# Optimization experiments

Hardware: AMD Instinct MI355X
Metric: run time of the kernel (lower is better)

The kernel has to match this reference:

```python
import jax, jax.numpy as jnp
import numpy as np

WD, WH, WW = 2, 7, 7          # window size (D, H, W)
SD, SH, SW = 1, 3, 3          # shift size
NUM_HEADS = 3
DIM = 96
N = WD * WH * WW              # tokens per window = 98


def _rel_pos_index():
    coords = np.stack(np.meshgrid(np.arange(WD), np.arange(WH), np.arange(WW), indexing='ij'))
    flat = coords.reshape(3, -1)                                   # (3, N)
    rel = (flat[:, :, None] - flat[:, None, :]).transpose(1, 2, 0)  # (N, N, 3)
    rel[..., 0] += WD - 1
    rel[..., 1] += WH - 1
    rel[..., 2] += WW - 1
    rel[..., 0] *= (2 * WH - 1) * (2 * WW - 1)
    rel[..., 1] *= (2 * WW - 1)
    return rel.sum(-1)                                             # (N, N) int


def _attn_mask(D, H, W):
    # shifted-window mask as in compute_mask(); purely shape-dependent constant
    img = np.zeros((D, H, W), np.float32)
    cnt = 0
    for d in (slice(-WD), slice(-WD, -SD), slice(-SD, None)):
        for h in (slice(-WH), slice(-WH, -SH), slice(-SH, None)):
            for w in (slice(-WW), slice(-WW, -SW), slice(-SW, None)):
                img[d, h, w] = cnt
                cnt += 1
    mw = img.reshape(D // WD, WD, H // WH, WH, W // WW, WW)
    mw = mw.transpose(0, 2, 4, 1, 3, 5).reshape(-1, N)             # (nW, N)
    diff = mw[:, None, :] - mw[:, :, None]
    return np.where(diff != 0, np.float32(-100.0), np.float32(0.0))  # (nW, N, N)


def _layernorm(x, w, b, eps=1e-5):
    mu = x.mean(-1, keepdims=True)
    var = ((x - mu) ** 2).mean(-1, keepdims=True)
    return (x - mu) * jax.lax.rsqrt(var + eps) * w + b


def _window_partition(x):
    B, D, H, W, C = x.shape
    x = x.reshape(B, D // WD, WD, H // WH, WH, W // WW, WW, C)
    return x.transpose(0, 1, 3, 5, 2, 4, 6, 7).reshape(-1, N, C)


def _window_reverse(win, B, D, H, W):
    C = win.shape[-1]
    x = win.reshape(B, D // WD, H // WH, W // WW, WD, WH, WW, C)
    return x.transpose(0, 1, 4, 2, 5, 3, 6, 7).reshape(B, D, H, W, C)


def swin_block(x, norm1_w, norm1_b, qkv_w, qkv_b, rpb_table, proj_w, proj_b,
               norm2_w, norm2_b, fc1_w, fc1_b, fc2_w, fc2_b):
    B, D, H, W, C = x.shape
    hd = C // NUM_HEADS
    shortcut = x
    # W-MSA (shifted) branch
    h = _layernorm(x, norm1_w, norm1_b)
    h = jnp.roll(h, shift=(-SD, -SH, -SW), axis=(1, 2, 3))
    win = _window_partition(h)                                     # (B*nW, N, C)
    qkv = win @ qkv_w.T + qkv_b                                    # (B*nW, N, 3C)
    qkv = qkv.reshape(-1, N, 3, NUM_HEADS, hd).transpose(2, 0, 3, 1, 4)
    q = qkv[0] * (hd ** -0.5)
    k, v = qkv[1], qkv[2]                                          # (B*nW, nh, N, hd)
    attn = jnp.einsum('whnd,whmd->whnm', q, k)                     # (B*nW, nh, N, N)
    rpi = jnp.asarray(_rel_pos_index().reshape(-1))
    bias = rpb_table[rpi].reshape(N, N, NUM_HEADS).transpose(2, 0, 1)
    attn = attn + bias[None]
    mask = jnp.asarray(_attn_mask(D, H, W))                        # (nW, N, N)
    nW = mask.shape[0]
    attn = attn.reshape(B, nW, NUM_HEADS, N, N) + mask[None, :, None]
    attn = jax.nn.softmax(attn.reshape(-1, NUM_HEADS, N, N), axis=-1)
    out = jnp.einsum('whnm,whmd->whnd', attn, v)                   # (B*nW, nh, N, hd)
    out = out.transpose(0, 2, 1, 3).reshape(-1, N, C)
    out = out @ proj_w.T + proj_b
    out = _window_reverse(out, B, D, H, W)
    out = jnp.roll(out, shift=(SD, SH, SW), axis=(1, 2, 3))
    x = shortcut + out
    # MLP branch
    h2 = _layernorm(x, norm2_w, norm2_b)
    h2 = jax.nn.gelu(h2 @ fc1_w.T + fc1_b, approximate=False) @ fc2_w.T + fc2_b
    return x + h2


def setup_inputs() -> dict:
    key = jax.random.key(0)
    ks = jax.random.split(key, 8)
    C, HID = DIM, 4 * DIM
    return {
        'x': jax.random.normal(ks[0], (2, 8, 112, 112, C), jnp.float32),
        'norm1_w': jnp.ones((C,), jnp.float32),
        'norm1_b': jnp.zeros((C,), jnp.float32),
        'qkv_w': jax.random.normal(ks[1], (3 * C, C), jnp.float32) * 0.02,
        'qkv_b': jnp.zeros((3 * C,), jnp.float32),
        'rpb_table': jax.random.normal(ks[2], ((2 * WD - 1) * (2 * WH - 1) * (2 * WW - 1), NUM_HEADS), jnp.float32) * 0.02,
        'proj_w': jax.random.normal(ks[3], (C, C), jnp.float32) * 0.02,
        'proj_b': jnp.zeros((C,), jnp.float32),
        'norm2_w': jnp.ones((C,), jnp.float32),
        'norm2_b': jnp.zeros((C,), jnp.float32),
        'fc1_w': jax.random.normal(ks[4], (HID, C), jnp.float32) * 0.02,
        'fc1_b': jnp.zeros((HID,), jnp.float32),
        'fc2_w': jax.random.normal(ks[5], (C, HID), jnp.float32) * 0.02,
        'fc2_b': jnp.zeros((C,), jnp.float32),
    }


def reference(x, norm1_w, norm1_b, qkv_w, qkv_b, rpb_table, proj_w, proj_b,
              norm2_w, norm2_b, fc1_w, fc1_b, fc2_w, fc2_b):
    return swin_block(x, norm1_w, norm1_b, qkv_w, qkv_b, rpb_table, proj_w, proj_b,
                      norm2_w, norm2_b, fc1_w, fc1_b, fc2_w, fc2_b)
```

## Files before the change

### kernel.cpp

```cpp
#include <hip/hip_runtime.h>
#include <hip/hip_bf16.h>


typedef __bf16 bf16x8 __attribute__((ext_vector_type(8)));
typedef __bf16 bf16x4 __attribute__((ext_vector_type(4)));
typedef float f32x4 __attribute__((ext_vector_type(4)));

#define SCALE_Q 0.17677669529663687f
#define LOG2E   1.4426950408889634f
#define SCALE_QE (SCALE_Q * LOG2E)

static __device__ __forceinline__ f32x4 mfma16(bf16x8 a, bf16x8 b, f32x4 c) {
  return __builtin_amdgcn_mfma_f32_16x16x32_bf16(a, b, c, 0, 0, 0);
}

static __device__ __forceinline__ float fast_exp2(float x) {
#if __has_builtin(__builtin_amdgcn_exp2f)
  return __builtin_amdgcn_exp2f(x);
#else
  return exp2f(x);
#endif
}
static __device__ __forceinline__ float fast_rcp(float x) {
#if __has_builtin(__builtin_amdgcn_rcpf)
  return __builtin_amdgcn_rcpf(x);
#else
  return 1.f / x;
#endif
}

static __device__ __forceinline__ float fast_gelu(float x) {
  float e = fast_exp2(x * fmaf(-0.1029445213f, x * x, -2.3022077385f));
  return x * fast_rcp(1.f + e);
}

static __device__ __forceinline__ int src_tok(int wi, int n) {
  int b = wi >> 10, r = wi & 1023;
  int d0 = r >> 8, h0 = (r >> 4) & 15, w0 = r & 15;
  int dd = n / 49, rem = n - dd * 49, hh = rem / 7, ww = rem - hh * 7;
  int d = (d0 * 2 + dd + 1) & 7;
  int h = h0 * 7 + hh + 3; if (h >= 112) h -= 112;
  int w = w0 * 7 + ww + 3; if (w >= 112) w -= 112;
  return ((b * 8 + d) * 112 + h) * 112 + w;
}

static __device__ __forceinline__ int region_cls(int cls, int n) {
  int dd = n / 49, rem = n - dd * 49, hh = rem / 7, ww = rem - hh * 7;
  int dr = (cls & 4) ? dd + 1 : 0;
  int hr = (cls & 2) ? (hh < 4 ? 1 : 2) : 0;
  int wr = (cls & 1) ? (ww < 4 ? 1 : 2) : 0;
  return dr * 9 + hr * 3 + wr;
}

__global__ __launch_bounds__(256) void k0_prep(
    const float* __restrict__ qkv_w, const float* __restrict__ qkv_b,
    const float* __restrict__ rpb, const float* __restrict__ proj_w,
    const float* __restrict__ fc1_w, const float* __restrict__ fc2_w,
    __bf16* __restrict__ wqkv, float* __restrict__ qkvb_s,
    __bf16* __restrict__ wproj, __bf16* __restrict__ wfc1, __bf16* __restrict__ wfc2,
    float* __restrict__ biasF) {
  int idx = blockIdx.x * 256 + threadIdx.x;
  if (idx < 27648) {
    int row = idx / 96; float v = qkv_w[idx];
    wqkv[idx] = (__bf16)(row < 96 ? v * SCALE_QE : v); return;
  }
  idx -= 27648;
  if (idx < 9216) { wproj[idx] = (__bf16)proj_w[idx]; return; }
  idx -= 9216;
  if (idx < 36864) { wfc1[idx] = (__bf16)fc1_w[idx]; return; }
  idx -= 36864;
  if (idx < 36864) { wfc2[idx] = (__bf16)fc2_w[idx]; return; }
  idx -= 36864;
  if (idx < 288) { float v = qkv_b[idx]; qkvb_s[idx] = idx < 96 ? v * SCALE_QE : v; return; }
  idx -= 288;
  if (idx < 301056) {
    int j = idx & 3, lane = (idx >> 2) & 63, t = idx >> 8;
    int nt = t % 7, mt = (t / 7) % 7, hd = (t / 49) % 3, cls = t / 147;
    int i = 16 * mt + 4 * (lane >> 4) + j;
    int jt = 16 * nt + (lane & 15);
    float v;
    if (jt >= 98) {
      v = -1e30f;
    } else {
      float rp = 0.f;
      if (i < 98) {
        int di = i / 49, ri_ = i - di * 49, hi = ri_ / 7, wi_ = ri_ - hi * 7;
        int dj = jt / 49, rj_ = jt - dj * 49, hj = rj_ / 7, wj = rj_ - hj * 7;
        int rpi = (di - dj + 1) * 169 + (hi - hj + 6) * 13 + (wi_ - wj + 6);
        rp = rpb[rpi * 3 + hd];
      }
      float mk = (region_cls(cls, i) != region_cls(cls, jt)) ? -100.f : 0.f;
      v = (rp + mk) * LOG2E;
    }
    biasF[idx] = v;
  }
}

__global__ __launch_bounds__(512, 1) void k1234_attn(
    const float* __restrict__ x, const float* __restrict__ n1w, const float* __restrict__ n1b,
    const __bf16* __restrict__ wqkv, const float* __restrict__ qkvb,
    const f32x4* __restrict__ biasF, const __bf16* __restrict__ wproj,
    const float* __restrict__ projb, float* __restrict__ x2) {
  int wi = blockIdx.x;
  int tid = threadIdx.x;
  int wave = tid >> 6, l = tid & 63, col = l & 15, gq = l >> 4;
  __shared__ __bf16 win_lds[112][104];
  __shared__ __bf16 Q_lds[112][104];
  __shared__ __bf16 K_lds[112][104];
  __shared__ __bf16 Vt_lds[96][136];
  __shared__ __bf16 p_lds[8][16][136];

  if (tid < 392) {
    int row = tid >> 2, cq = (tid & 3) * 24;
    const float* src = x + (size_t)src_tok(wi, row) * 96 + cq;
    float v[24];
    float sm = 0.f, sq = 0.f;
#pragma unroll
    for (int i = 0; i < 6; i++) {
      f32x4 u = *(const f32x4*)(src + 4 * i);
#pragma unroll
      for (int k = 0; k < 4; k++) { v[4 * i + k] = u[k]; sm += u[k]; sq += u[k] * u[k]; }
    }
    sm += __shfl_xor(sm, 1); sq += __shfl_xor(sq, 1);
    sm += __shfl_xor(sm, 2); sq += __shfl_xor(sq, 2);
    float mean = sm * (1.f / 96.f);
    float rstd = rsqrtf(sq * (1.f / 96.f) - mean * mean + 1e-5f);
    __bf16 outv[24];
#pragma unroll
    for (int i = 0; i < 24; i++)
      outv[i] = (__bf16)((v[i] - mean) * rstd * n1w[cq + i] + n1b[cq + i]);
#pragma unroll
    for (int i = 0; i < 3; i++)
      *(bf16x8*)&win_lds[row][cq + 8 * i] = *(bf16x8*)&outv[8 * i];
  } else {
    int z = tid - 392;
    for (int e = z; e < 1344; e += 120) { int r = e / 96; win_lds[98 + r][e - r * 96] = (__bf16)0.f; }
    for (int e = z; e < 1536; e += 120) Vt_lds[e >> 4][112 + (e & 15)] = (__bf16)0.f;
  }
  __syncthreads();

  if (wave < 6) {
    f32x4 acc[7][3] = {};
#pragma unroll
    for (int kk = 0; kk < 3; kk++) {
      bf16x8 a[7], bb[3];
#pragma unroll
      for (int mt = 0; mt < 7; mt++)
        a[mt] = *(const bf16x8*)&win_lds[16 * mt + col][32 * kk + 8 * gq];
#pragma unroll
      for (int t = 0; t < 3; t++)
        bb[t] = *(const bf16x8*)(wqkv + (size_t)(wave * 48 + 16 * t + col) * 96 + 32 * kk + 8 * gq);
#pragma unroll
      for (int mt = 0; mt < 7; mt++)
#pragma unroll
        for (int t = 0; t < 3; t++) acc[mt][t] = mfma16(a[mt], bb[t], acc[mt][t]);
    }
#pragma unroll
    for (int t = 0; t < 3; t++) {
      int n = wave * 48 + 16 * t + col;
      float bias = qkvb[n];
      int which = n / 96, c = n - which * 96;
      if (which == 2) {
#pragma unroll
        for (int mt = 0; mt < 7; mt++) {
          bf16x4 pk;
#pragma unroll
          for (int j = 0; j < 4; j++) pk[j] = (__bf16)(acc[mt][t][j] + bias);
          *(bf16x4*)&Vt_lds[c][16 * mt + 4 * gq] = pk;
        }
      } else {
#pragma unroll
        for (int mt = 0; mt < 7; mt++) {
#pragma unroll
          for (int j = 0; j < 4; j++) {
            int row = 16 * mt + 4 * gq + j;
            float v = acc[mt][t][j] + bias;
            if (which == 0) Q_lds[row][c] = (__bf16)v;
            else            K_lds[row][c] = (__bf16)v;
          }
        }
      }
    }
  }
  __syncthreads();

  {
    {
      int rr = l >> 2, cc = 112 + ((l & 3) << 2);
      *(uint2*)&p_lds[wave][rr][cc] = make_uint2(0u, 0u);
    }
    int cls = ((((wi >> 8) & 3) == 3) ? 4 : 0) | ((((wi >> 4) & 15) == 15) ? 2 : 0) |
              (((wi & 15) == 15) ? 1 : 0);
    int ntiles = (wave < 6) ? 3 : (wave == 6 ? 2 : 1);
    bf16x8 kf[7], vf[2][4];
    int cur_hd = -1;
#pragma unroll 1
    for (int s = 0; s < ntiles; s++) {
      int hd, mt;
      if (wave < 6)      { hd = wave >> 1; mt = ((wave & 1) ? 4 : 0) + s; }
      else if (wave == 6){ hd = s;         mt = 3; }
      else               { hd = 2;         mt = 3; }
      if (hd != cur_hd) {
        cur_hd = hd;
#pragma unroll
        for (int nt = 0; nt < 7; nt++)
          kf[nt] = *(const bf16x8*)&K_lds[16 * nt + col][hd * 32 + 8 * gq];
#pragma unroll
        for (int nt = 0; nt < 2; nt++)
#pragma unroll
          for (int ks = 0; ks < 4; ks++)
            vf[nt][ks] = *(const bf16x8*)&Vt_lds[hd * 32 + 16 * nt + col][32 * ks + 8 * gq];
      }
      const f32x4* bfr = biasF + (size_t)((cls * 3 + hd) * 49) * 64 + l;
      bf16x8 qf = *(const bf16x8*)&Q_lds[16 * mt + col][hd * 32 + 8 * gq];
      float sum0 = 0.f, sum1 = 0.f, sum2 = 0.f, sum3 = 0.f;
#pragma unroll
      for (int nt = 0; nt < 7; nt++) {
        f32x4 sv = mfma16(qf, kf[nt], bfr[(mt * 7 + nt) * 64]);
        float e0 = fast_exp2(sv[0]); sum0 += e0;
        float e1 = fast_exp2(sv[1]); sum1 += e1;
        float e2 = fast_exp2(sv[2]); sum2 += e2;
        float e3 = fast_exp2(sv[3]); sum3 += e3;
        p_lds[wave][4 * gq + 0][16 * nt + col] = (__bf16)e0;
        p_lds[wave][4 * gq + 1][16 * nt + col] = (__bf16)e1;
        p_lds[wave][4 * gq + 2][16 * nt + col] = (__bf16)e2;
        p_lds[wave][4 * gq + 3][16 * nt + col] = (__bf16)e3;
      }
#pragma unroll
      for (int m = 1; m < 16; m <<= 1) {
        sum0 += __shfl_xor(sum0, m, 16);
        sum1 += __shfl_xor(sum1, m, 16);
        sum2 += __shfl_xor(sum2, m, 16);
        sum3 += __shfl_xor(sum3, m, 16);
      }
      f32x4 oacc0 = {}, oacc1 = {};
#pragma unroll
      for (int ks = 0; ks < 4; ks++) {
        bf16x8 pa = *(const bf16x8*)&p_lds[wave][col][32 * ks + 8 * gq];
        oacc0 = mfma16(pa, vf[0][ks], oacc0);
        oacc1 = mfma16(pa, vf[1][ks], oacc1);
      }
      float inv0 = fast_rcp(sum0), inv1 = fast_rcp(sum1), inv2 = fast_rcp(sum2), inv3 = fast_rcp(sum3);
      int ibase = 16 * mt + 4 * gq;
      win_lds[ibase + 0][hd * 32 + col]      = (__bf16)(oacc0[0] * inv0);
      win_lds[ibase + 1][hd * 32 + col]      = (__bf16)(oacc0[1] * inv1);
      win_lds[ibase + 2][hd * 32 + col]      = (__bf16)(oacc0[2] * inv2);
      win_lds[ibase + 3][hd * 32 + col]      = (__bf16)(oacc0[3] * inv3);
      win_lds[ibase + 0][hd * 32 + 16 + col] = (__bf16)(oacc1[0] * inv0);
      win_lds[ibase + 1][hd * 32 + 16 + col] = (__bf16)(oacc1[1] * inv1);
      win_lds[ibase + 2][hd * 32 + 16 + col] = (__bf16)(oacc1[2] * inv2);
      win_lds[ibase + 3][hd * 32 + 16 + col] = (__bf16)(oacc1[3] * inv3);
    }
  }
  __syncthreads();

  if (wave < 6) {
    f32x4 acc[7] = {};
#pragma unroll
    for (int kk = 0; kk < 3; kk++) {
      bf16x8 bb = *(const bf16x8*)(wproj + (size_t)(16 * wave + col) * 96 + 32 * kk + 8 * gq);
#pragma unroll
      for (int mt = 0; mt < 7; mt++) {
        bf16x8 a = *(const bf16x8*)&win_lds[16 * mt + col][32 * kk + 8 * gq];
        acc[mt] = mfma16(a, bb, acc[mt]);
      }
    }
    int c = 16 * wave + col;
    float pb = projb[c];
#pragma unroll
    for (int mt = 0; mt < 7; mt++) {
#pragma unroll
      for (int j = 0; j < 4; j++) {
        int i = 16 * mt + 4 * gq + j;
        if (i < 98) {
          size_t s = (size_t)src_tok(wi, i);
          x2[s * 96 + c] = x[s * 96 + c] + acc[mt][j] + pb;
        }
      }
    }
  }
}

__global__ __launch_bounds__(512, 2) void k567_mlp(
    const float* __restrict__ n2w, const float* __restrict__ n2b,
    const __bf16* __restrict__ wfc1, const float* __restrict__ fc1b,
    const __bf16* __restrict__ wfc2, const float* __restrict__ fc2b,
    float* __restrict__ x2) {
  int tid = threadIdx.x;
  int wave = tid >> 6, l = tid & 63, col = l & 15, gq = l >> 4;
  size_t rowbase = (size_t)blockIdx.x * 128 + wave * 16;
  __shared__ __bf16 wbuf[2][96][104];
  __shared__ __bf16 htl[8][16][104];

  bf16x8 afr[3];
  {
    float v[24];
    float sm = 0.f, sq = 0.f;
    const float* src = x2 + (rowbase + col) * 96 + 8 * gq;
#pragma unroll
    for (int kk = 0; kk < 3; kk++) {
      f32x4 u0 = *(const f32x4*)(src + 32 * kk);
      f32x4 u1 = *(const f32x4*)(src + 32 * kk + 4);
#pragma unroll
      for (int k = 0; k < 4; k++) {
        v[8 * kk + k] = u0[k];     sm += u0[k]; sq += u0[k] * u0[k];
        v[8 * kk + 4 + k] = u1[k]; sm += u1[k]; sq += u1[k] * u1[k];
      }
    }
    sm += __shfl_xor(sm, 16); sq += __shfl_xor(sq, 16);
    sm += __shfl_xor(sm, 32); sq += __shfl_xor(sq, 32);
    float mean = sm * (1.f / 96.f);
    float rstd = rsqrtf(sq * (1.f / 96.f) - mean * mean + 1e-5f);
#pragma unroll
    for (int kk = 0; kk < 3; kk++) {
      f32x4 w0 = *(const f32x4*)(n2w + 32 * kk + 8 * gq);
      f32x4 w1 = *(const f32x4*)(n2w + 32 * kk + 8 * gq + 4);
      f32x4 b0 = *(const f32x4*)(n2b + 32 * kk + 8 * gq);
      f32x4 b1 = *(const f32x4*)(n2b + 32 * kk + 8 * gq + 4);
#pragma unroll
      for (int k = 0; k < 4; k++) {
        afr[kk][k]     = (__bf16)((v[8 * kk + k]     - mean) * rstd * w0[k] + b0[k]);
        afr[kk][4 + k] = (__bf16)((v[8 * kk + 4 + k] - mean) * rstd * w1[k] + b1[k]);
      }
    }
  }

#define STAGE_LOAD(qq, st)                                                        \
  {                                                                               \
    _Pragma("unroll")                                                             \
    for (int i = 0; i < 4; i++) {                                                 \
      int u = tid + 512 * i;                                                      \
      int which = u >= 1152; int uu = u - which * 1152;                           \
      int row = uu / 12, c = uu - row * 12;                                       \
      const __bf16* g = which ? (wfc2 + (size_t)row * 384 + (qq) * 96 + c * 8)    \
                              : (wfc1 + ((size_t)((qq) * 96 + row)) * 96 + c * 8);\
      st[i] = *(const bf16x8*)g;                                                  \
    }                                                                             \
    if (tid < 256) {                                                              \
      int u = 2048 + tid;                                                         \
      int row = (u - 1152) / 12, c = (u - 1152) - row * 12;                       \
      st[4] = *(const bf16x8*)(wfc2 + (size_t)row * 384 + (qq) * 96 + c * 8);     \
    }                                                                             \
  }
#define STAGE_WRITE(st)                                                           \
  {                                                                               \
    _Pragma("unroll")                                                             \
    for (int i = 0; i < 4; i++) {                                                 \
      int u = tid + 512 * i;                                                      \
      int which = u >= 1152; int uu = u - which * 1152;                           \
      int row = uu / 12, c = uu - row * 12;                                       \
      *(bf16x8*)&wbuf[which][row][c * 8] = st[i];                                 \
    }                                                                             \
    if (tid < 256) {                                                              \
      int u = 2048 + tid;                                                         \
      int row = (u - 1152) / 12, c = (u - 1152) - row * 12;                       \
      *(bf16x8*)&wbuf[1][row][c * 8] = st[4];                                     \
    }                                                                             \
  }

  {
    bf16x8 st[5];
    STAGE_LOAD(0, st);
    STAGE_WRITE(st);
  }
  __syncthreads();

  f32x4 oc[6] = {};
#pragma unroll 1
  for (int q = 0; q < 4; q++) {
    bf16x8 st[5];
    if (q < 3) STAGE_LOAD(q + 1, st);
    f32x4 acc[6] = {};
#pragma unroll
    for (int kk = 0; kk < 3; kk++) {
      bf16x8 bb[6];
#pragma unroll
      for (int t = 0; t < 6; t++)
        bb[t] = *(const bf16x8*)&wbuf[0][16 * t + col][32 * kk + 8 * gq];
#pragma unroll
      for (int t = 0; t < 6; t++) acc[t] = mfma16(afr[kk], bb[t], acc[t]);
    }
#pragma unroll
    for (int t = 0; t < 6; t++) {
      float bv = fc1b[q * 96 + 16 * t + col];
#pragma unroll
      for (int j = 0; j < 4; j++)
        htl[wave][4 * gq + j][16 * t + col] = (__bf16)fast_gelu(acc[t][j] + bv);
    }
#pragma unroll
    for (int kk = 0; kk < 3; kk++) {
      bf16x8 a0 = *(const bf16x8*)&htl[wave][col][32 * kk + 8 * gq];
      bf16x8 bb[6];
#pragma unroll
      for (int t = 0; t < 6; t++)
        bb[t] = *(const bf16x8*)&wbuf[1][16 * t + col][32 * kk + 8 * gq];
#pragma unroll
      for (int t = 0; t < 6; t++) oc[t] = mfma16(a0, bb[t], oc[t]);
    }
    __syncthreads();
    if (q < 3) {
      STAGE_WRITE(st);
      __syncthreads();
    }
  }
#pragma unroll
  for (int t = 0; t < 6; t++) {
    float bv = fc2b[16 * t + col];
#pragma unroll
    for (int j = 0; j < 4; j++) {
      size_t row = rowbase + 4 * gq + j;
      x2[row * 96 + 16 * t + col] = x2[row * 96 + 16 * t + col] + oc[t][j] + bv;
    }
  }
#undef STAGE_LOAD
#undef STAGE_WRITE
}

#define O_WQKV   0L
#define O_WPROJ  55296L
#define O_WFC1   73728L
#define O_WFC2   147456L
#define O_QKVB   221184L
#define O_BIASF  222336L

extern "C" void kernel_launch(void* const* d_in, const int* in_sizes, int n_in,
                              void* d_out, int out_size, void* d_ws, size_t ws_size,
                              hipStream_t stream) {
  const float* x     = (const float*)d_in[0];
  const float* n1w   = (const float*)d_in[1];
  const float* n1b   = (const float*)d_in[2];
  const float* qkvw  = (const float*)d_in[3];
  const float* qkvb  = (const float*)d_in[4];
  const float* rpb   = (const float*)d_in[5];
  const float* projw = (const float*)d_in[6];
  const float* projb = (const float*)d_in[7];
  const float* n2w   = (const float*)d_in[8];
  const float* n2b   = (const float*)d_in[9];
  const float* fc1w  = (const float*)d_in[10];
  const float* fc1b  = (const float*)d_in[11];
  const float* fc2w  = (const float*)d_in[12];
  const float* fc2b  = (const float*)d_in[13];

  char* ws = (char*)d_ws;
  __bf16* wqkv   = (__bf16*)(ws + O_WQKV);
  __bf16* wproj  = (__bf16*)(ws + O_WPROJ);
  __bf16* wfc1   = (__bf16*)(ws + O_WFC1);
  __bf16* wfc2   = (__bf16*)(ws + O_WFC2);
  float*  qkvb_s = (float*)(ws + O_QKVB);
  float*  biasF  = (float*)(ws + O_BIASF);
  float*  x2     = (float*)d_out;

  k0_prep<<<1610, 256, 0, stream>>>(qkvw, qkvb, rpb, projw, fc1w, fc2w,
                                    wqkv, qkvb_s, wproj, wfc1, wfc2, biasF);
  k1234_attn<<<2048, 512, 0, stream>>>(x, n1w, n1b, wqkv, qkvb_s,
                                       (const f32x4*)biasF, wproj, projb, x2);
  k567_mlp<<<1568, 512, 0, stream>>>(n2w, n2b, wfc1, fc1b, wfc2, fc2b, x2);
}
```

Measured before the change: 182.0 us.

## Transpose MFMA operands for vectorized Q/K stores and stage proj output for coalesced residual writes

```diff
diff --git a/kernel.cpp b/kernel.cpp
--- a/kernel.cpp
+++ b/kernel.cpp
@@ -105,10 +105,12 @@
   int tid = threadIdx.x;
   int wave = tid >> 6, l = tid & 63, col = l & 15, gq = l >> 4;
   __shared__ __bf16 win_lds[112][104];
-  __shared__ __bf16 Q_lds[112][104];
-  __shared__ __bf16 K_lds[112][104];
+  __shared__ __align__(16) __bf16 QK_lds[2][112][104];
   __shared__ __bf16 Vt_lds[96][136];
   __shared__ __bf16 p_lds[8][16][136];
+  auto& Q_lds = QK_lds[0];
+  auto& K_lds = QK_lds[1];
+  float (*stage)[100] = (float(*)[100])QK_lds;
 
   if (tid < 392) {
     int row = tid >> 2, cq = (tid & 3) * 24;
@@ -141,6 +143,7 @@
 
   if (wave < 6) {
     f32x4 acc[7][3] = {};
+    bool isQK = (wave < 4);
 #pragma unroll
     for (int kk = 0; kk < 3; kk++) {
       bf16x8 a[7], bb[3];
@@ -153,31 +156,38 @@
 #pragma unroll
       for (int mt = 0; mt < 7; mt++)
 #pragma unroll
-        for (int t = 0; t < 3; t++) acc[mt][t] = mfma16(a[mt], bb[t], acc[mt][t]);
-    }
-#pragma unroll
-    for (int t = 0; t < 3; t++) {
-      int n = wave * 48 + 16 * t + col;
-      float bias = qkvb[n];
-      int which = n / 96, c = n - which * 96;
-      if (which == 2) {
+        for (int t = 0; t < 3; t++)
+          acc[mt][t] = isQK ? mfma16(bb[t], a[mt], acc[mt][t])
+                            : mfma16(a[mt], bb[t], acc[mt][t]);
+    }
+    if (isQK) {
+#pragma unroll
+      for (int t = 0; t < 3; t++) {
+        int nb = wave * 48 + 16 * t + 4 * gq;
+        f32x4 b4 = *(const f32x4*)(qkvb + nb);
+        int isK = nb >= 96;
+        int cb = nb - (isK ? 96 : 0);
 #pragma unroll
         for (int mt = 0; mt < 7; mt++) {
           bf16x4 pk;
 #pragma unroll
+          for (int j = 0; j < 4; j++) pk[j] = (__bf16)(acc[mt][t][j] + b4[j]);
+          if (isK) *(bf16x4*)&K_lds[16 * mt + col][cb] = pk;
+          else     *(bf16x4*)&Q_lds[16 * mt + col][cb] = pk;
+        }
+      }
+    } else {
+#pragma unroll
+      for (int t = 0; t < 3; t++) {
+        int n = wave * 48 + 16 * t + col;
+        float bias = qkvb[n];
+        int c = n - 192;
+#pragma unroll
+        for (int mt = 0; mt < 7; mt++) {
+          bf16x4 pk;
+#pragma unroll
           for (int j = 0; j < 4; j++) pk[j] = (__bf16)(acc[mt][t][j] + bias);
           *(bf16x4*)&Vt_lds[c][16 * mt + 4 * gq] = pk;
-        }
-      } else {
-#pragma unroll
-        for (int mt = 0; mt < 7; mt++) {
-#pragma unroll
-          for (int j = 0; j < 4; j++) {
-            int row = 16 * mt + 4 * gq + j;
-            float v = acc[mt][t][j] + bias;
-            if (which == 0) Q_lds[row][c] = (__bf16)v;
-            else            K_lds[row][c] = (__bf16)v;
-          }
         }
       }
     }
@@ -262,21 +272,33 @@
 #pragma unroll
       for (int mt = 0; mt < 7; mt++) {
         bf16x8 a = *(const bf16x8*)&win_lds[16 * mt + col][32 * kk + 8 * gq];
-        acc[mt] = mfma16(a, bb, acc[mt]);
-      }
-    }
-    int c = 16 * wave + col;
-    float pb = projb[c];
+        acc[mt] = mfma16(bb, a, acc[mt]);
+      }
+    }
+    f32x4 pb4 = *(const f32x4*)(projb + 16 * wave + 4 * gq);
 #pragma unroll
     for (int mt = 0; mt < 7; mt++) {
-#pragma unroll
-      for (int j = 0; j < 4; j++) {
-        int i = 16 * mt + 4 * gq + j;
-        if (i < 98) {
-          size_t s = (size_t)src_tok(wi, i);
-          x2[s * 96 + c] = x[s * 96 + c] + acc[mt][j] + pb;
-        }
-      }
+      f32x4 o;
+#pragma unroll
+      for (int j = 0; j < 4; j++) o[j] = acc[mt][j] + pb4[j];
+      *(f32x4*)&stage[16 * mt + col][16 * wave + 4 * gq] = o;
+    }
+  }
+  __syncthreads();
+
+  if (tid < 392) {
+    int row = tid >> 2, cq = (tid & 3) * 24;
+    size_t s = (size_t)src_tok(wi, row);
+    const float* xs = x + s * 96 + cq;
+    float* xd = x2 + s * 96 + cq;
+#pragma unroll
+    for (int i = 0; i < 6; i++) {
+      f32x4 u = *(const f32x4*)(xs + 4 * i);
+      f32x4 st = *(const f32x4*)&stage[row][cq + 4 * i];
+      f32x4 r;
+#pragma unroll
+      for (int k = 0; k < 4; k++) r[k] = u[k] + st[k];
+      *(f32x4*)(xd + 4 * i) = r;
     }
   }
 }
```

Measured after the change: 201.0 us. 10.5% more time.
